# Performance work log

Hardware: AMD Instinct MI355X
Metric: run time of the kernel (lower is better)

Reference implementation:

```python
import jax, jax.numpy as jnp
import numpy as np

N_EXPERTS = 8
D_IN = 512
D_OUT = 512


def setup_inputs() -> dict:
    key = jax.random.key(0)
    k1, k2, k3, k4 = jax.random.split(key, 4)
    B, N = 16, 4096
    z = jax.random.randint(k1, (B, N), 0, N_EXPERTS, dtype=jnp.int64 if jax.config.jax_enable_x64 else jnp.int32)
    x = jax.random.normal(k2, (B, N, D_IN), dtype=jnp.float32)
    # Expert parameters: map_list[e] modeled as Linear(D_IN, D_OUT)
    W = jax.random.normal(k3, (N_EXPERTS, D_IN, D_OUT), dtype=jnp.float32) * (1.0 / np.sqrt(D_IN))
    b = jax.random.normal(k4, (N_EXPERTS, D_OUT), dtype=jnp.float32) * 0.01
    return {"z": z, "x": x, "W": W, "b": b}


def reference(z, x, W, b):
    B, N = z.shape
    z_flat = z.reshape(-1)                 # [T]
    x_flat = x.reshape(-1, x.shape[-1])    # [T, D_in]
    T = z_flat.shape[0]
    y = jnp.zeros((T, D_OUT), dtype=x.dtype)
    # Dense equivalent of mask-gather -> expert apply -> masked scatter.
    # Tokens with id == -1 (or any id not hit) stay zero, matching the torch code.
    for e in range(N_EXPERTS):
        mask = (z_flat == e)[:, None]      # [T, 1]
        y_e = x_flat @ W[e] + b[e]         # [T, D_out]
        y = jnp.where(mask, y_e, y)
    y = y.reshape(B, N, D_OUT)
    return (z, y)
```

## Files before the change

### kernel.cpp

```cpp
#include <hip/hip_runtime.h>
#include <stdint.h>

#define NEXP 8
#define DD   512
#define BM   64
#define BN   512

typedef short s16x8 __attribute__((ext_vector_type(8)));
typedef float f32x4 __attribute__((ext_vector_type(4)));

static __device__ __forceinline__ unsigned short f2bf(float f) {
    union { float f; unsigned u; } v; v.f = f;
    unsigned r = v.u + 0x7FFFu + ((v.u >> 16) & 1u);
    return (unsigned short)(r >> 16);
}


__global__ void hist_kernel(const int* __restrict__ z, int* __restrict__ counts, int T) {
    __shared__ int lc[NEXP];
    int tid = threadIdx.x;
    if (tid < NEXP) lc[tid] = 0;
    __syncthreads();
    int t = blockIdx.x * blockDim.x + tid;
    if (t < T) atomicAdd(&lc[z[t]], 1);
    __syncthreads();
    if (tid < NEXP) atomicAdd(&counts[tid], lc[tid]);
}

__global__ void scan_kernel(const int* __restrict__ counts, int* __restrict__ cursors,
                            int4* __restrict__ table, int max_tiles) {
    __shared__ int off[NEXP + 1];
    __shared__ int tb[NEXP + 1];
    int tid = threadIdx.x;
    if (tid == 0) {
        int o = 0, tbs = 0;
        for (int e = 0; e < NEXP; e++) {
            off[e] = o; tb[e] = tbs;
            cursors[e] = o;
            int c = counts[e];
            o += c;
            tbs += (c + BM - 1) / BM;
        }
        off[NEXP] = o; tb[NEXP] = tbs;
    }
    __syncthreads();
    for (int idx = tid; idx < max_tiles; idx += blockDim.x) {
        int4 ent; ent.x = -1; ent.y = 0; ent.z = 0; ent.w = 0;
#pragma unroll
        for (int e = 0; e < NEXP; e++) {
            if (idx >= tb[e] && idx < tb[e + 1]) {
                int r = (idx - tb[e]) * BM;
                ent.x = e; ent.y = off[e] + r; ent.z = (off[e + 1] - off[e]) - r;
            }
        }
        table[idx] = ent;
    }
}

__global__ void scatter_kernel(const int* __restrict__ z, int* __restrict__ cursors,
                               int* __restrict__ token_index, float* __restrict__ zout, int T) {
    __shared__ int lc[NEXP];
    __shared__ int lbase[NEXP];
    int tid = threadIdx.x;
    if (tid < NEXP) lc[tid] = 0;
    __syncthreads();
    int t = blockIdx.x * blockDim.x + tid;
    int e = 0, rank = 0;
    if (t < T) {
        e = z[t];
        rank = atomicAdd(&lc[e], 1);
        zout[t] = (float)e;
    }
    __syncthreads();
    if (tid < NEXP) lbase[tid] = atomicAdd(&cursors[tid], lc[tid]);
    __syncthreads();
    if (t < T) token_index[lbase[e] + rank] = t;
}

__global__ void convw_kernel(const float* __restrict__ W, unsigned short* __restrict__ Wt) {
    __shared__ float tile[32][33];
    int e = blockIdx.z, k0 = blockIdx.x * 32, n0 = blockIdx.y * 32;
    int tid = threadIdx.x;
    const float* We = W + (size_t)e * DD * DD;
    unsigned short* WtE = Wt + (size_t)e * DD * DD;
    int c = tid & 31, r0 = tid >> 5;
#pragma unroll
    for (int i = 0; i < 4; i++) {
        int kr = r0 + 8 * i;
        tile[kr][c] = We[(size_t)(k0 + kr) * DD + n0 + c];
    }
    __syncthreads();
#pragma unroll
    for (int i = 0; i < 4; i++) {
        int nr = r0 + 8 * i;
        WtE[(size_t)(n0 + nr) * DD + k0 + c] = f2bf(tile[c][nr]);
    }
}


__global__ __launch_bounds__(512, 4) void gemm3_kernel(
    const float* __restrict__ x,
    const unsigned short* __restrict__ Wt,
    const float* __restrict__ bias,
    const int* __restrict__ token_index,
    const int4* __restrict__ table,
    float* __restrict__ y)
{
    int4 te = table[blockIdx.x];
    const int e = te.x;
    if (e < 0) return;
    const int base = te.y;
    const int rows_valid = te.z < BM ? te.z : BM;

    __shared__ unsigned short Als[BM * 64];
    __shared__ unsigned short Bls[BN * 64];

    const int tid  = threadIdx.x;
    const int lane = tid & 63;
    const int wave = tid >> 6;
    const int wn   = wave * 64;

    const int ra  = tid >> 3;
    const int ca  = tid & 7;
    const int gca = ca ^ (ra & 7);

    const int rr  = (ra < rows_valid) ? ra : 0;
    const int tok = token_index[base + rr];
    const float* asrc = x + (size_t)tok * DD + gca * 8;

    const unsigned short* WtE  = Wt + (size_t)e * DD * DD;
    const unsigned short* bsrc = WtE + (size_t)ra * DD + gca * 8;

    f32x4 acc[4][4];
#pragma unroll
    for (int i = 0; i < 4; i++)
#pragma unroll
        for (int j = 0; j < 4; j++) acc[i][j] = (f32x4){0.f, 0.f, 0.f, 0.f};

    const int quad = lane >> 4;
    const int lrow = lane & 15;

    float4 av0 = *(const float4*)(asrc);
    float4 av1 = *(const float4*)(asrc + 4);

    for (int k0 = 0; k0 < DD; k0 += 64) {
        __syncthreads();
        uint4 p;
        p.x = (unsigned)f2bf(av0.x) | ((unsigned)f2bf(av0.y) << 16);
        p.y = (unsigned)f2bf(av0.z) | ((unsigned)f2bf(av0.w) << 16);
        p.z = (unsigned)f2bf(av1.x) | ((unsigned)f2bf(av1.y) << 16);
        p.w = (unsigned)f2bf(av1.z) | ((unsigned)f2bf(av1.w) << 16);
        *(uint4*)(&Als[tid * 8]) = p;
#pragma unroll
        for (int j = 0; j < 8; j++) {
            const unsigned short* gb = bsrc + (size_t)j * 64 * DD + k0;
            unsigned short* lb = &Bls[(size_t)(tid + j * 512) * 8];
            __builtin_amdgcn_global_load_lds((const __attribute__((address_space(1))) void*)gb,
                                             (__attribute__((address_space(3))) void*)lb, 16, 0, 0);
        }
        if (k0 + 64 < DD) {
            av0 = *(const float4*)(asrc + k0 + 64);
            av1 = *(const float4*)(asrc + k0 + 68);
        }
        __syncthreads();

#pragma unroll
        for (int ks = 0; ks < 2; ks++) {
            s16x8 af[4], bq[4];
#pragma unroll
            for (int i = 0; i < 4; i++) {
                int r = i * 16 + lrow;
                af[i] = *(const s16x8*)(&Als[r * 64 + (((quad + 4 * ks) ^ (r & 7)) * 8)]);
            }
#pragma unroll
            for (int j = 0; j < 4; j++) {
                int n = wn + j * 16 + lrow;
                bq[j] = *(const s16x8*)(&Bls[n * 64 + (((quad + 4 * ks) ^ (n & 7)) * 8)]);
            }
#pragma unroll
            for (int i = 0; i < 4; i++)
#pragma unroll
                for (int j = 0; j < 4; j++)
                    acc[i][j] = __builtin_amdgcn_mfma_f32_16x16x32_bf16(af[i], bq[j], acc[i][j], 0, 0, 0);
        }
    }

    const int lcol = lane & 15;
    float bv[4];
#pragma unroll
    for (int j = 0; j < 4; j++) bv[j] = bias[e * DD + wn + j * 16 + lcol];
#pragma unroll
    for (int i = 0; i < 4; i++) {
#pragma unroll
        for (int reg = 0; reg < 4; reg++) {
            int r = i * 16 + quad * 4 + reg;
            if (r < rows_valid) {
                int t = token_index[base + r];
                float* yr = y + (size_t)t * DD + wn + lcol;
#pragma unroll
                for (int j = 0; j < 4; j++)
                    yr[j * 16] = acc[i][j][reg] + bv[j];
            }
        }
    }
}


extern "C" void kernel_launch(void* const* d_in, const int* in_sizes, int n_in,
                              void* d_out, int out_size, void* d_ws, size_t ws_size,
                              hipStream_t stream) {
    const int*   z = (const int*)d_in[0];
    const float* x = (const float*)d_in[1];
    const float* W = (const float*)d_in[2];
    const float* b = (const float*)d_in[3];
    const int T = in_sizes[0];

    float* zout = (float*)d_out;
    float* y    = (float*)d_out + T;

    char* ws = (char*)d_ws;
    int*  counts      = (int*)ws;
    int*  cursors     = (int*)(ws + 64);
    int4* table       = (int4*)(ws + 256);
    int*  token_index = (int*)(ws + 17408);
    unsigned short* Wt = (unsigned short*)(ws + 279552);

    const int max_tiles = T / BM + NEXP;

    hipMemsetAsync(ws, 0, 64, stream);
    hist_kernel<<<(T + 255) / 256, 256, 0, stream>>>(z, counts, T);
    convw_kernel<<<dim3(DD / 32, DD / 32, NEXP), 256, 0, stream>>>(W, Wt);
    scan_kernel<<<1, 256, 0, stream>>>(counts, cursors, table, max_tiles);
    scatter_kernel<<<(T + 255) / 256, 256, 0, stream>>>(z, cursors, token_index, zout, T);
    gemm3_kernel<<<dim3(max_tiles), 512, 0, stream>>>(x, Wt, b, token_index, table, y);
}
```

Before: 309.9 us.

## Stage full A tile in LDS once and read B fragments directly from global

The GEMM kernel now converts and stores the entire 64x512 bf16 activation tile into shared memory up front, with a single barrier, removing the per-k-step barriers. Weight fragments are loaded straight from global memory (via L2) into registers for the MFMA instead of being staged through LDS with global_load_lds. This drops the B LDS buffer and the sync overhead, but exposes global-load latency inside the MFMA loop without software prefetch. Each wave's B loads are strided 16-byte accesses across rows.

```diff
diff --git a/kernel.cpp b/kernel.cpp
--- a/kernel.cpp
+++ b/kernel.cpp
@@ -98,7 +98,7 @@
 }
 
 
-__global__ __launch_bounds__(512, 4) void gemm3_kernel(
+__global__ __launch_bounds__(512, 4) void gemm4_kernel(
     const float* __restrict__ x,
     const unsigned short* __restrict__ Wt,
     const float* __restrict__ bias,
@@ -112,8 +112,7 @@
     const int base = te.y;
     const int rows_valid = te.z < BM ? te.z : BM;
 
-    __shared__ unsigned short Als[BM * 64];
-    __shared__ unsigned short Bls[BN * 64];
+    __shared__ unsigned short Als[BM * DD];
 
     const int tid  = threadIdx.x;
     const int lane = tid & 63;
@@ -128,8 +127,18 @@
     const int tok = token_index[base + rr];
     const float* asrc = x + (size_t)tok * DD + gca * 8;
 
-    const unsigned short* WtE  = Wt + (size_t)e * DD * DD;
-    const unsigned short* bsrc = WtE + (size_t)ra * DD + gca * 8;
+#pragma unroll
+    for (int s = 0; s < 8; s++) {
+        float4 v0 = *(const float4*)(asrc + s * 64);
+        float4 v1 = *(const float4*)(asrc + s * 64 + 4);
+        uint4 p;
+        p.x = (unsigned)f2bf(v0.x) | ((unsigned)f2bf(v0.y) << 16);
+        p.y = (unsigned)f2bf(v0.z) | ((unsigned)f2bf(v0.w) << 16);
+        p.z = (unsigned)f2bf(v1.x) | ((unsigned)f2bf(v1.y) << 16);
+        p.w = (unsigned)f2bf(v1.z) | ((unsigned)f2bf(v1.w) << 16);
+        *(uint4*)(&Als[s * 4096 + tid * 8]) = p;
+    }
+    __syncthreads();
 
     f32x4 acc[4][4];
 #pragma unroll
@@ -140,43 +149,22 @@
     const int quad = lane >> 4;
     const int lrow = lane & 15;
 
-    float4 av0 = *(const float4*)(asrc);
-    float4 av1 = *(const float4*)(asrc + 4);
-
+    const unsigned short* bbase = Wt + (size_t)e * DD * DD + (size_t)(wn + lrow) * DD + quad * 8;
+
+#pragma unroll 2
     for (int k0 = 0; k0 < DD; k0 += 64) {
-        __syncthreads();
-        uint4 p;
-        p.x = (unsigned)f2bf(av0.x) | ((unsigned)f2bf(av0.y) << 16);
-        p.y = (unsigned)f2bf(av0.z) | ((unsigned)f2bf(av0.w) << 16);
-        p.z = (unsigned)f2bf(av1.x) | ((unsigned)f2bf(av1.y) << 16);
-        p.w = (unsigned)f2bf(av1.z) | ((unsigned)f2bf(av1.w) << 16);
-        *(uint4*)(&Als[tid * 8]) = p;
-#pragma unroll
-        for (int j = 0; j < 8; j++) {
-            const unsigned short* gb = bsrc + (size_t)j * 64 * DD + k0;
-            unsigned short* lb = &Bls[(size_t)(tid + j * 512) * 8];
-            __builtin_amdgcn_global_load_lds((const __attribute__((address_space(1))) void*)gb,
-                                             (__attribute__((address_space(3))) void*)lb, 16, 0, 0);
-        }
-        if (k0 + 64 < DD) {
-            av0 = *(const float4*)(asrc + k0 + 64);
-            av1 = *(const float4*)(asrc + k0 + 68);
-        }
-        __syncthreads();
-
+        const int sblk = (k0 >> 6) * 4096;
 #pragma unroll
         for (int ks = 0; ks < 2; ks++) {
             s16x8 af[4], bq[4];
 #pragma unroll
             for (int i = 0; i < 4; i++) {
                 int r = i * 16 + lrow;
-                af[i] = *(const s16x8*)(&Als[r * 64 + (((quad + 4 * ks) ^ (r & 7)) * 8)]);
+                af[i] = *(const s16x8*)(&Als[sblk + r * 64 + (((quad + 4 * ks) ^ (r & 7)) * 8)]);
             }
 #pragma unroll
-            for (int j = 0; j < 4; j++) {
-                int n = wn + j * 16 + lrow;
-                bq[j] = *(const s16x8*)(&Bls[n * 64 + (((quad + 4 * ks) ^ (n & 7)) * 8)]);
-            }
+            for (int j = 0; j < 4; j++)
+                bq[j] = *(const s16x8*)(bbase + (size_t)j * 16 * DD + k0 + ks * 32);
 #pragma unroll
             for (int i = 0; i < 4; i++)
 #pragma unroll
@@ -232,5 +220,5 @@
     convw_kernel<<<dim3(DD / 32, DD / 32, NEXP), 256, 0, stream>>>(W, Wt);
     scan_kernel<<<1, 256, 0, stream>>>(counts, cursors, table, max_tiles);
     scatter_kernel<<<(T + 255) / 256, 256, 0, stream>>>(z, cursors, token_index, zout, T);
-    gemm3_kernel<<<dim3(max_tiles), 512, 0, stream>>>(x, Wt, b, token_index, table, y);
-}
+    gemm4_kernel<<<dim3(max_tiles), 512, 0, stream>>>(x, Wt, b, token_index, table, y);
+}
```

Result: slower. 328.9 us (+6.2%).

## Retile grouped GEMM to 128x128, fuse prep kernels, drop scan table

Applied to the files above, without the earlier changes.

Changes the GEMM tile from 64 tokens by 512 outputs to 128 by 128, spreading work across a 2D grid of 256-thread blocks. Each block now derives its expert and row range from the counts itself, so the separate scan/table kernel goes away. The weight conversion and histogram are merged into one launch, and the scatter kernel computes offsets inline. A packed bf16 convert instruction and nontemporal output stores are also added. The trade-off is that each x row is now gathered and converted four times, once per output-column block.

```diff
diff --git a/kernel.cpp b/kernel.cpp
--- a/kernel.cpp
+++ b/kernel.cpp
@@ -3,8 +3,8 @@
 
 #define NEXP 8
 #define DD   512
-#define BM   64
-#define BN   512
+#define BM   128
+#define BN   128
 
 typedef short s16x8 __attribute__((ext_vector_type(8)));
 typedef float f32x4 __attribute__((ext_vector_type(4)));
@@ -15,54 +15,66 @@
     return (unsigned short)(r >> 16);
 }
 
-
-__global__ void hist_kernel(const int* __restrict__ z, int* __restrict__ counts, int T) {
+static __device__ __forceinline__ unsigned cvtpk(float lo, float hi) {
+    unsigned r;
+    asm("v_cvt_pk_bf16_f32 %0, %1, %2" : "=v"(r) : "v"(lo), "v"(hi));
+    return r;
+}
+
+
+__global__ __launch_bounds__(256) void prep1_kernel(const float* __restrict__ W,
+                                                    unsigned short* __restrict__ Wt,
+                                                    const int* __restrict__ z,
+                                                    int* __restrict__ counts, int T) {
+    const int bx = blockIdx.x;
+    const int tid = threadIdx.x;
+    if (bx < 2048) {
+        __shared__ float tile[32][33];
+        const int e = bx >> 8;
+        const int b = bx & 255;
+        const int k0 = (b & 15) * 32;
+        const int n0 = (b >> 4) * 32;
+        const float* We = W + (size_t)e * DD * DD;
+        unsigned short* WtE = Wt + (size_t)e * DD * DD;
+        const int c = tid & 31, r0 = tid >> 5;
+#pragma unroll
+        for (int i = 0; i < 4; i++) {
+            int kr = r0 + 8 * i;
+            tile[kr][c] = We[(size_t)(k0 + kr) * DD + n0 + c];
+        }
+        __syncthreads();
+#pragma unroll
+        for (int i = 0; i < 4; i++) {
+            int nr = r0 + 8 * i;
+            WtE[(size_t)(n0 + nr) * DD + k0 + c] = f2bf(tile[c][nr]);
+        }
+    } else {
+        __shared__ int lc[NEXP];
+        if (tid < NEXP) lc[tid] = 0;
+        __syncthreads();
+        int t = (bx - 2048) * 256 + tid;
+        if (t < T) atomicAdd(&lc[z[t]], 1);
+        __syncthreads();
+        if (tid < NEXP) atomicAdd(&counts[tid], lc[tid]);
+    }
+}
+
+
+__global__ __launch_bounds__(256) void scatter_kernel(const int* __restrict__ z,
+                                                      const int* __restrict__ counts,
+                                                      int* __restrict__ cursors,
+                                                      int* __restrict__ token_index,
+                                                      float* __restrict__ zout, int T) {
     __shared__ int lc[NEXP];
-    int tid = threadIdx.x;
+    __shared__ int off[NEXP];
+    __shared__ int lbase[NEXP];
+    const int tid = threadIdx.x;
     if (tid < NEXP) lc[tid] = 0;
-    __syncthreads();
-    int t = blockIdx.x * blockDim.x + tid;
-    if (t < T) atomicAdd(&lc[z[t]], 1);
-    __syncthreads();
-    if (tid < NEXP) atomicAdd(&counts[tid], lc[tid]);
-}
-
-__global__ void scan_kernel(const int* __restrict__ counts, int* __restrict__ cursors,
-                            int4* __restrict__ table, int max_tiles) {
-    __shared__ int off[NEXP + 1];
-    __shared__ int tb[NEXP + 1];
-    int tid = threadIdx.x;
     if (tid == 0) {
-        int o = 0, tbs = 0;
-        for (int e = 0; e < NEXP; e++) {
-            off[e] = o; tb[e] = tbs;
-            cursors[e] = o;
-            int c = counts[e];
-            o += c;
-            tbs += (c + BM - 1) / BM;
-        }
-        off[NEXP] = o; tb[NEXP] = tbs;
-    }
-    __syncthreads();
-    for (int idx = tid; idx < max_tiles; idx += blockDim.x) {
-        int4 ent; ent.x = -1; ent.y = 0; ent.z = 0; ent.w = 0;
-#pragma unroll
-        for (int e = 0; e < NEXP; e++) {
-            if (idx >= tb[e] && idx < tb[e + 1]) {
-                int r = (idx - tb[e]) * BM;
-                ent.x = e; ent.y = off[e] + r; ent.z = (off[e + 1] - off[e]) - r;
-            }
-        }
-        table[idx] = ent;
-    }
-}
-
-__global__ void scatter_kernel(const int* __restrict__ z, int* __restrict__ cursors,
-                               int* __restrict__ token_index, float* __restrict__ zout, int T) {
-    __shared__ int lc[NEXP];
-    __shared__ int lbase[NEXP];
-    int tid = threadIdx.x;
-    if (tid < NEXP) lc[tid] = 0;
+        int o = 0;
+#pragma unroll
+        for (int e = 0; e < NEXP; e++) { off[e] = o; o += counts[e]; }
+    }
     __syncthreads();
     int t = blockIdx.x * blockDim.x + tid;
     int e = 0, rank = 0;
@@ -72,64 +84,60 @@
         zout[t] = (float)e;
     }
     __syncthreads();
-    if (tid < NEXP) lbase[tid] = atomicAdd(&cursors[tid], lc[tid]);
+    if (tid < NEXP) lbase[tid] = off[tid] + atomicAdd(&cursors[tid], lc[tid]);
     __syncthreads();
     if (t < T) token_index[lbase[e] + rank] = t;
 }
 
-__global__ void convw_kernel(const float* __restrict__ W, unsigned short* __restrict__ Wt) {
-    __shared__ float tile[32][33];
-    int e = blockIdx.z, k0 = blockIdx.x * 32, n0 = blockIdx.y * 32;
-    int tid = threadIdx.x;
-    const float* We = W + (size_t)e * DD * DD;
-    unsigned short* WtE = Wt + (size_t)e * DD * DD;
-    int c = tid & 31, r0 = tid >> 5;
-#pragma unroll
-    for (int i = 0; i < 4; i++) {
-        int kr = r0 + 8 * i;
-        tile[kr][c] = We[(size_t)(k0 + kr) * DD + n0 + c];
-    }
-    __syncthreads();
-#pragma unroll
-    for (int i = 0; i < 4; i++) {
-        int nr = r0 + 8 * i;
-        WtE[(size_t)(n0 + nr) * DD + k0 + c] = f2bf(tile[c][nr]);
-    }
-}
-
-
-__global__ __launch_bounds__(512, 4) void gemm3_kernel(
+
+__global__ __launch_bounds__(256) void gemm5_kernel(
     const float* __restrict__ x,
     const unsigned short* __restrict__ Wt,
     const float* __restrict__ bias,
     const int* __restrict__ token_index,
-    const int4* __restrict__ table,
+    const int* __restrict__ counts,
     float* __restrict__ y)
 {
-    int4 te = table[blockIdx.x];
-    const int e = te.x;
-    if (e < 0) return;
-    const int base = te.y;
-    const int rows_valid = te.z < BM ? te.z : BM;
-
     __shared__ unsigned short Als[BM * 64];
     __shared__ unsigned short Bls[BN * 64];
-
-    const int tid  = threadIdx.x;
+    __shared__ int meta[3];
+
+    const int tid = threadIdx.x;
+    if (tid == 0) {
+        int o = 0, tb = 0, e = -1, base = 0, rows = 0;
+#pragma unroll
+        for (int ee = 0; ee < NEXP; ee++) {
+            int c = counts[ee];
+            int nt = (c + BM - 1) >> 7;
+            int ib = (int)blockIdx.x - tb;
+            if (ib >= 0 && ib < nt) { e = ee; base = o + (ib << 7); rows = c - (ib << 7); }
+            o += c; tb += nt;
+        }
+        meta[0] = e; meta[1] = base; meta[2] = rows < BM ? rows : BM;
+    }
+    __syncthreads();
+    const int e = meta[0];
+    if (e < 0) return;
+    const int base = meta[1];
+    const int rows_valid = meta[2];
+    const int n0 = blockIdx.y * BN;
+
     const int lane = tid & 63;
     const int wave = tid >> 6;
-    const int wn   = wave * 64;
-
-    const int ra  = tid >> 3;
-    const int ca  = tid & 7;
-    const int gca = ca ^ (ra & 7);
-
-    const int rr  = (ra < rows_valid) ? ra : 0;
-    const int tok = token_index[base + rr];
-    const float* asrc = x + (size_t)tok * DD + gca * 8;
-
-    const unsigned short* WtE  = Wt + (size_t)e * DD * DD;
-    const unsigned short* bsrc = WtE + (size_t)ra * DD + gca * 8;
+    const int wm = (wave & 1) * 64;
+    const int wn = (wave >> 1) * 64;
+
+    int srow[4], sgc[4];
+    const float* aptr[4];
+#pragma unroll
+    for (int q = 0; q < 4; q++) {
+        int s = wave * 256 + q * 64 + lane;
+        srow[q] = s >> 3;
+        sgc[q]  = (s & 7) ^ ((s >> 3) & 7);
+        int rr = srow[q] < rows_valid ? srow[q] : rows_valid - 1;
+        aptr[q] = x + (size_t)token_index[base + rr] * DD + sgc[q] * 8;
+    }
+    const unsigned short* WtE = Wt + (size_t)e * DD * DD;
 
     f32x4 acc[4][4];
 #pragma unroll
@@ -140,27 +148,29 @@
     const int quad = lane >> 4;
     const int lrow = lane & 15;
 
-    float4 av0 = *(const float4*)(asrc);
-    float4 av1 = *(const float4*)(asrc + 4);
-
     for (int k0 = 0; k0 < DD; k0 += 64) {
         __syncthreads();
-        uint4 p;
-        p.x = (unsigned)f2bf(av0.x) | ((unsigned)f2bf(av0.y) << 16);
-        p.y = (unsigned)f2bf(av0.z) | ((unsigned)f2bf(av0.w) << 16);
-        p.z = (unsigned)f2bf(av1.x) | ((unsigned)f2bf(av1.y) << 16);
-        p.w = (unsigned)f2bf(av1.z) | ((unsigned)f2bf(av1.w) << 16);
-        *(uint4*)(&Als[tid * 8]) = p;
-#pragma unroll
-        for (int j = 0; j < 8; j++) {
-            const unsigned short* gb = bsrc + (size_t)j * 64 * DD + k0;
-            unsigned short* lb = &Bls[(size_t)(tid + j * 512) * 8];
+#pragma unroll
+        for (int q = 0; q < 4; q++) {
+            const unsigned short* gb = WtE + (size_t)(n0 + srow[q]) * DD + k0 + sgc[q] * 8;
+            unsigned short* lb = &Bls[(size_t)(wave * 256 + q * 64) * 8];
             __builtin_amdgcn_global_load_lds((const __attribute__((address_space(1))) void*)gb,
                                              (__attribute__((address_space(3))) void*)lb, 16, 0, 0);
         }
-        if (k0 + 64 < DD) {
-            av0 = *(const float4*)(asrc + k0 + 64);
-            av1 = *(const float4*)(asrc + k0 + 68);
+        float4 va[4][2];
+#pragma unroll
+        for (int q = 0; q < 4; q++) {
+            va[q][0] = *(const float4*)(aptr[q] + k0);
+            va[q][1] = *(const float4*)(aptr[q] + k0 + 4);
+        }
+#pragma unroll
+        for (int q = 0; q < 4; q++) {
+            uint4 p;
+            p.x = cvtpk(va[q][0].x, va[q][0].y);
+            p.y = cvtpk(va[q][0].z, va[q][0].w);
+            p.z = cvtpk(va[q][1].x, va[q][1].y);
+            p.w = cvtpk(va[q][1].z, va[q][1].w);
+            *(uint4*)(&Als[(size_t)(wave * 256 + q * 64 + lane) * 8]) = p;
         }
         __syncthreads();
 
@@ -169,13 +179,13 @@
             s16x8 af[4], bq[4];
 #pragma unroll
             for (int i = 0; i < 4; i++) {
-                int r = i * 16 + lrow;
+                int r = wm + i * 16 + lrow;
                 af[i] = *(const s16x8*)(&Als[r * 64 + (((quad + 4 * ks) ^ (r & 7)) * 8)]);
             }
 #pragma unroll
             for (int j = 0; j < 4; j++) {
-                int n = wn + j * 16 + lrow;
-                bq[j] = *(const s16x8*)(&Bls[n * 64 + (((quad + 4 * ks) ^ (n & 7)) * 8)]);
+                int r = wn + j * 16 + lrow;
+                bq[j] = *(const s16x8*)(&Bls[r * 64 + (((quad + 4 * ks) ^ (r & 7)) * 8)]);
             }
 #pragma unroll
             for (int i = 0; i < 4; i++)
@@ -188,18 +198,18 @@
     const int lcol = lane & 15;
     float bv[4];
 #pragma unroll
-    for (int j = 0; j < 4; j++) bv[j] = bias[e * DD + wn + j * 16 + lcol];
+    for (int j = 0; j < 4; j++) bv[j] = bias[e * DD + n0 + wn + j * 16 + lcol];
 #pragma unroll
     for (int i = 0; i < 4; i++) {
 #pragma unroll
         for (int reg = 0; reg < 4; reg++) {
-            int r = i * 16 + quad * 4 + reg;
+            int r = wm + i * 16 + quad * 4 + reg;
             if (r < rows_valid) {
                 int t = token_index[base + r];
-                float* yr = y + (size_t)t * DD + wn + lcol;
+                float* yr = y + (size_t)t * DD + n0 + wn + lcol;
 #pragma unroll
                 for (int j = 0; j < 4; j++)
-                    yr[j * 16] = acc[i][j][reg] + bv[j];
+                    __builtin_nontemporal_store(acc[i][j][reg] + bv[j], yr + j * 16);
             }
         }
     }
@@ -221,16 +231,14 @@
     char* ws = (char*)d_ws;
     int*  counts      = (int*)ws;
     int*  cursors     = (int*)(ws + 64);
-    int4* table       = (int4*)(ws + 256);
     int*  token_index = (int*)(ws + 17408);
     unsigned short* Wt = (unsigned short*)(ws + 279552);
 
     const int max_tiles = T / BM + NEXP;
-
-    hipMemsetAsync(ws, 0, 64, stream);
-    hist_kernel<<<(T + 255) / 256, 256, 0, stream>>>(z, counts, T);
-    convw_kernel<<<dim3(DD / 32, DD / 32, NEXP), 256, 0, stream>>>(W, Wt);
-    scan_kernel<<<1, 256, 0, stream>>>(counts, cursors, table, max_tiles);
-    scatter_kernel<<<(T + 255) / 256, 256, 0, stream>>>(z, cursors, token_index, zout, T);
-    gemm3_kernel<<<dim3(max_tiles), 512, 0, stream>>>(x, Wt, b, token_index, table, y);
-}
+    const int hist_blocks = (T + 255) / 256;
+
+    hipMemsetAsync(ws, 0, 128, stream);
+    prep1_kernel<<<2048 + hist_blocks, 256, 0, stream>>>(W, Wt, z, counts, T);
+    scatter_kernel<<<hist_blocks, 256, 0, stream>>>(z, counts, cursors, token_index, zout, T);
+    gemm5_kernel<<<dim3(max_tiles, DD / BN), 256, 0, stream>>>(x, Wt, b, token_index, counts, y);
+}
```

After: 327.3 us. 5.6% more time.
